# Kernel tuning notes

Hardware: AMD Instinct MI355X
Metric: run time of the kernel (lower is better)

## Reference

```python
import jax, jax.numpy as jnp
import numpy as np

N_NODES = 1_000_000
N_EDGES = 16_000_000
D = 2          # num_dimensions (hard-coded in source)
H = 64         # hidden_channnels
G = 1024       # number of graphs in the batch


def setup_inputs() -> dict:
    key = jax.random.key(0)
    ks = jax.random.split(key, 10)
    x = jax.random.normal(ks[0], (N_NODES, D), dtype=jnp.float32)
    edge_index = jax.random.randint(ks[1], (2, N_EDGES), 0, N_NODES, dtype=jnp.int64)
    batch = jnp.sort(jax.random.randint(ks[2], (N_NODES,), 0, G, dtype=jnp.int64))
    s = 0.5
    return {
        "x": x,
        "lin_w": jax.random.normal(ks[3], (D, D), dtype=jnp.float32) * s,
        "lin_b": jnp.zeros((D,), jnp.float32),
        "gn_weight": jnp.ones((D,), jnp.float32),
        "gn_bias": jnp.zeros((D,), jnp.float32),
        "gn_mean_scale": jnp.ones((D,), jnp.float32),
        "gcn_w": jax.random.normal(ks[4], (D, D), dtype=jnp.float32) * s,
        "gcn_b": jnp.zeros((D,), jnp.float32),
        "fc1_w": jax.random.normal(ks[5], (H, D), dtype=jnp.float32) * s,
        "fc1_b": jnp.zeros((H,), jnp.float32),
        "fc2_w": jax.random.normal(ks[6], (D, H), dtype=jnp.float32) * (1.0 / np.sqrt(H)),
        "fc2_b": jnp.zeros((D,), jnp.float32),
        "edge_index": edge_index,
        "batch": batch,
    }


def reference(x, lin_w, lin_b, gn_weight, gn_bias, gn_mean_scale,
              gcn_w, gcn_b, fc1_w, fc1_b, fc2_w, fc2_b, edge_index, batch):
    n = x.shape[0]
    # lin
    h = x @ lin_w.T + lin_b
    # GraphNorm called without batch -> single-graph stats; eps = num_dimensions = 2 (arg-order quirk)
    mean = h.mean(axis=0)
    out = h - mean * gn_mean_scale
    var = (out * out).mean(axis=0)
    h = gn_weight * out * jax.lax.rsqrt(var + jnp.float32(D)) + gn_bias
    h = jax.nn.relu(h)
    # GCNConv (add_self_loops=True, sym norm) + residual
    row, col = edge_index[0], edge_index[1]
    deg = jax.ops.segment_sum(jnp.ones_like(col, dtype=h.dtype), col, num_segments=n) + 1.0
    dis = jax.lax.rsqrt(deg)                       # deg^{-1/2}
    hw = h @ gcn_w.T                               # [N, D]
    msg = (dis[row] * dis[col])[:, None] * hw[row] # [E, D]
    agg = jax.ops.segment_sum(msg, col, num_segments=n)
    conv = agg + hw / deg[:, None] + gcn_b         # self-loop term = dis_i^2 * hw_i
    h = conv + h
    # fc1
    h = h @ fc1_w.T + fc1_b                        # [N, H]
    # InstanceNorm1d on 2D input -> unbatched (C=N, L=H): per-row norm over H; eps = H (arg-order quirk)
    m = h.mean(axis=1, keepdims=True)
    v = ((h - m) ** 2).mean(axis=1, keepdims=True)
    h = (h - m) * jax.lax.rsqrt(v + jnp.float32(H))
    # fc2
    h = h @ fc2_w.T + fc2_b                        # [N, D]
    # scatter_mean over batch
    ssum = jax.ops.segment_sum(h, batch, num_segments=G)
    cnt = jax.ops.segment_sum(jnp.ones((n,), h.dtype), batch, num_segments=G)
    return ssum / jnp.maximum(cnt, 1.0)[:, None]
```

## Files before the change

kernel.cpp:

```cpp
#include <hip/hip_runtime.h>

#define BLK 256
#define CH 8192
#define BSHIFT 11
#define BRANGE 2048
#define BMASK 2047
#define NSB 512


__global__ void k_stats(const float* __restrict__ x, int n, double* __restrict__ partials) {
    float s0 = 0.f, s1 = 0.f, s2 = 0.f, s3 = 0.f, s4 = 0.f;
    int nv = n >> 1;
    int stride = gridDim.x * blockDim.x;
    for (int i = blockIdx.x * blockDim.x + threadIdx.x; i < nv; i += stride) {
        float4 v = reinterpret_cast<const float4*>(x)[i];
        s0 += v.x + v.z; s1 += v.y + v.w;
        s2 += v.x * v.x + v.z * v.z;
        s3 += v.y * v.y + v.w * v.w;
        s4 += v.x * v.y + v.z * v.w;
    }
    if (blockIdx.x == 0 && threadIdx.x == 0 && (n & 1)) {
        float2 v = reinterpret_cast<const float2*>(x)[n - 1];
        s0 += v.x; s1 += v.y; s2 += v.x * v.x; s3 += v.y * v.y; s4 += v.x * v.y;
    }
    for (int off = 32; off; off >>= 1) {
        s0 += __shfl_down(s0, off);
        s1 += __shfl_down(s1, off);
        s2 += __shfl_down(s2, off);
        s3 += __shfl_down(s3, off);
        s4 += __shfl_down(s4, off);
    }
    __shared__ double lds[4][5];
    int wid = threadIdx.x >> 6;
    if ((threadIdx.x & 63) == 0) {
        lds[wid][0] = s0; lds[wid][1] = s1; lds[wid][2] = s2;
        lds[wid][3] = s3; lds[wid][4] = s4;
    }
    __syncthreads();
    if (threadIdx.x == 0) {
        double t0 = 0, t1 = 0, t2 = 0, t3 = 0, t4 = 0;
        for (int w = 0; w < 4; ++w) {
            t0 += lds[w][0]; t1 += lds[w][1]; t2 += lds[w][2];
            t3 += lds[w][3]; t4 += lds[w][4];
        }
        double* o = partials + (size_t)blockIdx.x * 5;
        o[0] = t0; o[1] = t1; o[2] = t2; o[3] = t3; o[4] = t4;
    }
}


__global__ void k_params(const double* __restrict__ partials, int np,
                         const int* __restrict__ bhist, int NB,
                         int* __restrict__ gbase, int* __restrict__ cursor,
                         const float* lin_w, const float* lin_b,
                         const float* gn_w, const float* gn_b, const float* gn_ms,
                         const float* gcn_w, const float* gcn_b,
                         const float* fc1_w, const float* fc1_b,
                         const float* fc2_w, const float* fc2_b,
                         int n, float* __restrict__ P) {
    int tid = threadIdx.x;
    if (bhist) {
        __shared__ int si[256];
        int v0 = (2 * tid     < NB) ? bhist[2 * tid]     : 0;
        int v1 = (2 * tid + 1 < NB) ? bhist[2 * tid + 1] : 0;
        si[tid] = v0 + v1; __syncthreads();
        for (int off = 1; off < 256; off <<= 1) {
            int t = (tid >= off) ? si[tid - off] : 0;
            __syncthreads();
            si[tid] += t;
            __syncthreads();
        }
        int base = si[tid] - v0 - v1;
        if (2 * tid < NB)     { gbase[2 * tid]     = base;      cursor[2 * tid]     = base; }
        if (2 * tid + 1 < NB) { gbase[2 * tid + 1] = base + v0; cursor[2 * tid + 1] = base + v0; }
        if (tid == 255) gbase[NB] = si[255];
        __syncthreads();
    }
    double a0 = 0, a1 = 0, a2 = 0, a3 = 0, a4 = 0;
    for (int i = tid; i < np; i += blockDim.x) {
        const double* q = partials + (size_t)i * 5;
        a0 += q[0]; a1 += q[1]; a2 += q[2]; a3 += q[3]; a4 += q[4];
    }
    for (int off = 32; off; off >>= 1) {
        a0 += __shfl_down(a0, off);
        a1 += __shfl_down(a1, off);
        a2 += __shfl_down(a2, off);
        a3 += __shfl_down(a3, off);
        a4 += __shfl_down(a4, off);
    }
    __shared__ double red[4][5];
    int wid = tid >> 6;
    if ((tid & 63) == 0) {
        red[wid][0] = a0; red[wid][1] = a1; red[wid][2] = a2;
        red[wid][3] = a3; red[wid][4] = a4;
    }
    __syncthreads();
    if (tid != 0) return;
    double Sx0 = 0, Sx1 = 0, Sxx = 0, Syy = 0, Sxy = 0;
    for (int w = 0; w < 4; ++w) {
        Sx0 += red[w][0]; Sx1 += red[w][1]; Sxx += red[w][2];
        Syy += red[w][3]; Sxy += red[w][4];
    }
    double N = (double)n;
    for (int c = 0; c < 2; ++c) {
        double L0 = lin_w[c * 2], L1 = lin_w[c * 2 + 1], lb = lin_b[c];
        double m   = (L0 * Sx0 + L1 * Sx1) / N + lb;
        double Eh2 = (L0 * L0 * Sxx + L1 * L1 * Syy + 2.0 * L0 * L1 * Sxy
                      + 2.0 * lb * (L0 * Sx0 + L1 * Sx1)) / N + lb * lb;
        double s   = gn_ms[c];
        double var = Eh2 - 2.0 * s * m * m + s * s * m * m;
        double inv = 1.0 / sqrt(var + 2.0);
        double gam = gn_w[c];
        P[c * 2 + 0] = (float)(gam * inv * L0);
        P[c * 2 + 1] = (float)(gam * inv * L1);
        P[4 + c]     = (float)(gam * inv * (lb - m * s) + gn_b[c]);
    }
    P[6] = gcn_w[0]; P[7] = gcn_w[1]; P[8] = gcn_w[2]; P[9] = gcn_w[3];
    P[10] = gcn_b[0]; P[11] = gcn_b[1];
    double b0 = 0, b1 = 0, bb = 0;
    for (int j = 0; j < 64; ++j) { b0 += fc1_w[2 * j]; b1 += fc1_w[2 * j + 1]; bb += fc1_b[j]; }
    b0 /= 64.0; b1 /= 64.0; bb /= 64.0;
    double S00 = 0, S01 = 0, S11 = 0, Sb0 = 0, Sb1 = 0, Sbb = 0;
    double M00 = 0, M01 = 0, M10 = 0, M11 = 0, t0 = 0, t1 = 0;
    for (int j = 0; j < 64; ++j) {
        double w0 = fc1_w[2 * j] - b0, w1 = fc1_w[2 * j + 1] - b1, b = fc1_b[j] - bb;
        S00 += w0 * w0; S01 += w0 * w1; S11 += w1 * w1;
        Sb0 += w0 * b;  Sb1 += w1 * b;  Sbb += b * b;
        double f0 = fc2_w[j], f1 = fc2_w[64 + j];
        M00 += f0 * w0; M01 += f0 * w1; t0 += f0 * b;
        M10 += f1 * w0; M11 += f1 * w1; t1 += f1 * b;
    }
    P[12] = (float)(S00 / 64.0); P[13] = (float)(S01 / 64.0); P[14] = (float)(S11 / 64.0);
    P[15] = (float)(Sb0 / 64.0); P[16] = (float)(Sb1 / 64.0); P[17] = (float)(Sbb / 64.0);
    P[18] = (float)M00; P[19] = (float)M01; P[20] = (float)M10; P[21] = (float)M11;
    P[22] = (float)t0;  P[23] = (float)t1;
    P[24] = fc2_b[0];   P[25] = fc2_b[1];
}


__global__ void k_hist(const int* __restrict__ col, int E, int NB, int* __restrict__ bhist) {
    __shared__ int h[512];
    for (int j = threadIdx.x; j < 512; j += blockDim.x) h[j] = 0;
    __syncthreads();
    int nq = E >> 2;
    int stride = gridDim.x * blockDim.x;
    for (int q = blockIdx.x * blockDim.x + threadIdx.x; q < nq; q += stride) {
        int4 c = reinterpret_cast<const int4*>(col)[q];
        atomicAdd(&h[c.x >> BSHIFT], 1);
        atomicAdd(&h[c.y >> BSHIFT], 1);
        atomicAdd(&h[c.z >> BSHIFT], 1);
        atomicAdd(&h[c.w >> BSHIFT], 1);
    }
    if (blockIdx.x == 0) {
        for (int e = (nq << 2) + threadIdx.x; e < E; e += blockDim.x)
            atomicAdd(&h[col[e] >> BSHIFT], 1);
    }
    __syncthreads();
    for (int j = threadIdx.x; j < NB; j += blockDim.x)
        if (h[j]) atomicAdd(&bhist[j], h[j]);
}

__global__ __launch_bounds__(256) void k_binA(const int* __restrict__ row,
                                              const int* __restrict__ col, int E,
                                              int NB, int* __restrict__ cursor,
                                              unsigned* __restrict__ staging) {
    __shared__ unsigned buf[CH];
    __shared__ int h[512], lpos[512], lcur[512];
    __shared__ int si[256];
    int tid = threadIdx.x;
    int start = blockIdx.x * CH;
    int end = start + CH; if (end > E) end = E;
    h[tid] = 0; h[tid + 256] = 0;
    __syncthreads();
    for (int e = start + tid; e < end; e += 256)
        atomicAdd(&h[col[e] >> BSHIFT], 1);
    __syncthreads();
    int v0 = h[2 * tid], v1 = h[2 * tid + 1];
    si[tid] = v0 + v1; __syncthreads();
    for (int off = 1; off < 256; off <<= 1) {
        int t = (tid >= off) ? si[tid - off] : 0;
        __syncthreads();
        si[tid] += t;
        __syncthreads();
    }
    int base = si[tid] - v0 - v1;
    lpos[2 * tid]     = base;
    lpos[2 * tid + 1] = base + v0;
    lcur[2 * tid]     = (2 * tid     < NB && v0) ? atomicAdd(&cursor[2 * tid],     v0) : 0;
    lcur[2 * tid + 1] = (2 * tid + 1 < NB && v1) ? atomicAdd(&cursor[2 * tid + 1], v1) : 0;
    __syncthreads();
    for (int e = start + tid; e < end; e += 256) {
        int c = col[e];
        unsigned w = ((unsigned)row[e] << BSHIFT) | (unsigned)(c & BMASK);
        int slot = atomicAdd(&lpos[c >> BSHIFT], 1);
        buf[slot] = w;
    }
    __syncthreads();
    int wid = tid >> 6, lane = tid & 63;
    for (int b = wid; b < NB; b += 4) {
        int m = h[b];
        if (!m) continue;
        int lb = lpos[b] - m;
        int g = lcur[b];
        for (int k = lane; k < m; k += 64)
            staging[g + k] = buf[lb + k];
    }
}

__global__ __launch_bounds__(1024) void k_degprep(const unsigned* __restrict__ staging,
                                                  const int* __restrict__ gbase,
                                                  const float* __restrict__ x,
                                                  const float* __restrict__ P,
                                                  int n, int* __restrict__ deg,
                                                  float2* __restrict__ p) {
    __shared__ int hist[BRANGE];
    int tid = threadIdx.x;
    for (int j = tid; j < BRANGE; j += 1024) hist[j] = 0;
    __syncthreads();
    int s = gbase[blockIdx.x], e = gbase[blockIdx.x + 1];
    int pre = (4 - (s & 3)) & 3; int cnt = e - s; if (pre > cnt) pre = cnt;
    for (int i = s + tid; i < s + pre; i += 1024)
        atomicAdd(&hist[staging[i] & BMASK], 1);
    int vs = s + pre;
    int nq = (e - vs) >> 2;
    const uint4* sv = reinterpret_cast<const uint4*>(staging + vs);
    for (int q = tid; q < nq; q += 1024) {
        uint4 w = sv[q];
        atomicAdd(&hist[w.x & BMASK], 1);
        atomicAdd(&hist[w.y & BMASK], 1);
        atomicAdd(&hist[w.z & BMASK], 1);
        atomicAdd(&hist[w.w & BMASK], 1);
    }
    for (int i = vs + (nq << 2) + tid; i < e; i += 1024)
        atomicAdd(&hist[staging[i] & BMASK], 1);
    __syncthreads();
    float A00 = P[0], A01 = P[1], A10 = P[2], A11 = P[3], q0 = P[4], q1 = P[5];
    float g00 = P[6], g01 = P[7], g10 = P[8], g11 = P[9];
    int nb = blockIdx.x << BSHIFT;
    int lim = n - nb; if (lim > BRANGE) lim = BRANGE;
    for (int j = tid; j < lim; j += 1024) {
        int d = hist[j];
        deg[nb + j] = d;
        float2 v = reinterpret_cast<const float2*>(x)[nb + j];
        float gg0 = fmaxf(fmaf(A00, v.x, fmaf(A01, v.y, q0)), 0.f);
        float gg1 = fmaxf(fmaf(A10, v.x, fmaf(A11, v.y, q1)), 0.f);
        float hw0 = g00 * gg0 + g01 * gg1;
        float hw1 = g10 * gg0 + g11 * gg1;
        float degf = (float)d + 1.0f;
        float dis = rsqrtf(degf);
        p[nb + j] = make_float2(dis * hw0, dis * hw1);
    }
}

__global__ __launch_bounds__(1024) void k_aggfin(
        const unsigned* __restrict__ staging, const int* __restrict__ gbase,
        const float2* __restrict__ p, const float* __restrict__ x,
        const int* __restrict__ deg, const int* __restrict__ batch,
        const float* __restrict__ Pp, int n,
        float* __restrict__ gsum, float* __restrict__ gcnt) {
    __shared__ float acc[2 * BRANGE];
    int tid = threadIdx.x;
    for (int j = tid; j < 2 * BRANGE; j += 1024) acc[j] = 0.f;
    __syncthreads();
    int s = gbase[blockIdx.x], e = gbase[blockIdx.x + 1];
    int cnt = e - s;
    int pre = (4 - (s & 3)) & 3; if (pre > cnt) pre = cnt;
    for (int i = s + tid; i < s + pre; i += 1024) {
        unsigned w = staging[i]; float2 pv = p[w >> BSHIFT];
        atomicAdd(&acc[2 * (w & BMASK)],     pv.x);
        atomicAdd(&acc[2 * (w & BMASK) + 1], pv.y);
    }
    int vs = s + pre;
    int nq = (e - vs) >> 2;
    const uint4* sv = reinterpret_cast<const uint4*>(staging + vs);
    #pragma unroll 4
    for (int q = tid; q < nq; q += 1024) {
        uint4 w = sv[q];
        float2 p0 = p[w.x >> BSHIFT], p1 = p[w.y >> BSHIFT];
        float2 p2 = p[w.z >> BSHIFT], p3 = p[w.w >> BSHIFT];
        atomicAdd(&acc[2 * (w.x & BMASK)],     p0.x);
        atomicAdd(&acc[2 * (w.x & BMASK) + 1], p0.y);
        atomicAdd(&acc[2 * (w.y & BMASK)],     p1.x);
        atomicAdd(&acc[2 * (w.y & BMASK) + 1], p1.y);
        atomicAdd(&acc[2 * (w.z & BMASK)],     p2.x);
        atomicAdd(&acc[2 * (w.z & BMASK) + 1], p2.y);
        atomicAdd(&acc[2 * (w.w & BMASK)],     p3.x);
        atomicAdd(&acc[2 * (w.w & BMASK) + 1], p3.y);
    }
    for (int i = vs + (nq << 2) + tid; i < e; i += 1024) {
        unsigned w = staging[i]; float2 pv = p[w >> BSHIFT];
        atomicAdd(&acc[2 * (w & BMASK)],     pv.x);
        atomicAdd(&acc[2 * (w & BMASK) + 1], pv.y);
    }
    __syncthreads();

    float A00 = Pp[0], A01 = Pp[1], A10 = Pp[2], A11 = Pp[3], q0f = Pp[4], q1f = Pp[5];
    float g00 = Pp[6], g01 = Pp[7], g10 = Pp[8], g11 = Pp[9];
    float gb0 = Pp[10], gb1 = Pp[11];
    float S00 = Pp[12], S01 = Pp[13], S11 = Pp[14], Sb0 = Pp[15], Sb1 = Pp[16], Sbb = Pp[17];
    float M00 = Pp[18], M01 = Pp[19], M10 = Pp[20], M11 = Pp[21];
    float t0 = Pp[22], t1 = Pp[23], fb0 = Pp[24], fb1 = Pp[25];
    int nb = blockIdx.x << BSHIFT;
    int lim = n - nb; if (lim > BRANGE) lim = BRANGE;
    for (int j = tid; j < lim; j += 1024) {
        int i = nb + j;
        float2 v = reinterpret_cast<const float2*>(x)[i];
        float g0 = fmaxf(fmaf(A00, v.x, fmaf(A01, v.y, q0f)), 0.f);
        float g1 = fmaxf(fmaf(A10, v.x, fmaf(A11, v.y, q1f)), 0.f);
        float hw0 = g00 * g0 + g01 * g1;
        float hw1 = g10 * g0 + g11 * g1;
        float degf = (float)deg[i] + 1.0f;
        float dis = rsqrtf(degf);
        float a0v = acc[2 * j], a1v = acc[2 * j + 1];
        float c0 = dis * a0v + hw0 / degf + gb0 + g0;
        float c1 = dis * a1v + hw1 / degf + gb1 + g1;
        float vq = S00 * c0 * c0 + 2.f * S01 * c0 * c1 + S11 * c1 * c1
                 + 2.f * Sb0 * c0 + 2.f * Sb1 * c1 + Sbb;
        float inv = rsqrtf(vq + 64.0f);
        float o0 = inv * (M00 * c0 + M01 * c1 + t0) + fb0;
        float o1 = inv * (M10 * c0 + M11 * c1 + t1) + fb1;
        int bg = batch[i];
        unsigned long long act = __ballot(true);
        if (act == ~0ull) {
            int b0 = __shfl(bg, 0);
            if (__all(bg == b0)) {
                float s0 = o0, s1 = o1;
                for (int off = 32; off; off >>= 1) {
                    s0 += __shfl_down(s0, off);
                    s1 += __shfl_down(s1, off);
                }
                if ((tid & 63) == 0) {
                    atomicAdd(&gsum[2 * b0], s0);
                    atomicAdd(&gsum[2 * b0 + 1], s1);
                    atomicAdd(&gcnt[b0], 64.0f);
                }
            } else {
                atomicAdd(&gsum[2 * bg], o0);
                atomicAdd(&gsum[2 * bg + 1], o1);
                atomicAdd(&gcnt[bg], 1.0f);
            }
        } else {
            atomicAdd(&gsum[2 * bg], o0);
            atomicAdd(&gsum[2 * bg + 1], o1);
            atomicAdd(&gcnt[bg], 1.0f);
        }
    }
}

__global__ void k_div(const float* __restrict__ gsum, const float* __restrict__ gcnt,
                      float* __restrict__ out, int G) {
    int g = blockIdx.x * blockDim.x + threadIdx.x;
    if (g < G) {
        float c = fmaxf(gcnt[g], 1.0f);
        out[2 * g]     = gsum[2 * g] / c;
        out[2 * g + 1] = gsum[2 * g + 1] / c;
    }
}


__global__ void k_prep(const float* __restrict__ x, const int* __restrict__ deg,
                       const float* __restrict__ P, int n, float2* __restrict__ p) {
    int stride = gridDim.x * blockDim.x;
    float A00 = P[0], A01 = P[1], A10 = P[2], A11 = P[3], q0 = P[4], q1 = P[5];
    float g00 = P[6], g01 = P[7], g10 = P[8], g11 = P[9];
    for (int i = blockIdx.x * blockDim.x + threadIdx.x; i < n; i += stride) {
        float2 v = reinterpret_cast<const float2*>(x)[i];
        float g0 = fmaxf(fmaf(A00, v.x, fmaf(A01, v.y, q0)), 0.f);
        float g1 = fmaxf(fmaf(A10, v.x, fmaf(A11, v.y, q1)), 0.f);
        float hw0 = g00 * g0 + g01 * g1;
        float hw1 = g10 * g0 + g11 * g1;
        float degf = (float)deg[i] + 1.0f;
        float dis = rsqrtf(degf);
        p[i] = make_float2(dis * hw0, dis * hw1);
    }
}

__global__ void k_deg(const int* __restrict__ col, int E, int* __restrict__ deg) {
    int nq = (E + 3) >> 2;
    int q = blockIdx.x * blockDim.x + threadIdx.x;
    if (q >= nq) return;
    int base = q << 2;
    if (base + 3 < E) {
        int4 c = reinterpret_cast<const int4*>(col)[q];
        atomicAdd(&deg[c.x], 1); atomicAdd(&deg[c.y], 1);
        atomicAdd(&deg[c.z], 1); atomicAdd(&deg[c.w], 1);
    } else {
        for (int e = base; e < E; ++e) atomicAdd(&deg[col[e]], 1);
    }
}

__global__ void k_edge(const int* __restrict__ row, const int* __restrict__ col, int E,
                       const float2* __restrict__ p, float* __restrict__ agg) {
    int nq = (E + 3) >> 2;
    int q = blockIdx.x * blockDim.x + threadIdx.x;
    if (q >= nq) return;
    int base = q << 2;
    if (base + 3 < E) {
        int4 r = reinterpret_cast<const int4*>(row)[q];
        int4 c = reinterpret_cast<const int4*>(col)[q];
        float2 p0 = p[r.x], p1 = p[r.y], p2 = p[r.z], p3 = p[r.w];
        atomicAdd(&agg[2 * c.x], p0.x); atomicAdd(&agg[2 * c.x + 1], p0.y);
        atomicAdd(&agg[2 * c.y], p1.x); atomicAdd(&agg[2 * c.y + 1], p1.y);
        atomicAdd(&agg[2 * c.z], p2.x); atomicAdd(&agg[2 * c.z + 1], p2.y);
        atomicAdd(&agg[2 * c.w], p3.x); atomicAdd(&agg[2 * c.w + 1], p3.y);
    } else {
        for (int e = base; e < E; ++e) {
            float2 pv = p[row[e]];
            atomicAdd(&agg[2 * col[e]], pv.x);
            atomicAdd(&agg[2 * col[e] + 1], pv.y);
        }
    }
}

__global__ void k_final(const float* __restrict__ x, const int* __restrict__ deg,
                        const float* __restrict__ agg, const int* __restrict__ batch,
                        const float* __restrict__ P, int n,
                        float* __restrict__ gsum, float* __restrict__ gcnt) {
    int i = blockIdx.x * blockDim.x + threadIdx.x;
    bool valid = i < n;
    float A00 = P[0], A01 = P[1], A10 = P[2], A11 = P[3], q0 = P[4], q1 = P[5];
    float g00 = P[6], g01 = P[7], g10 = P[8], g11 = P[9];
    float gb0 = P[10], gb1 = P[11];
    float S00 = P[12], S01 = P[13], S11 = P[14], Sb0 = P[15], Sb1 = P[16], Sbb = P[17];
    float M00 = P[18], M01 = P[19], M10 = P[20], M11 = P[21];
    float t0 = P[22], t1 = P[23], fb0 = P[24], fb1 = P[25];

    float o0 = 0.f, o1 = 0.f;
    int b = 0;
    if (valid) {
        float2 v = reinterpret_cast<const float2*>(x)[i];
        float g0 = fmaxf(fmaf(A00, v.x, fmaf(A01, v.y, q0)), 0.f);
        float g1 = fmaxf(fmaf(A10, v.x, fmaf(A11, v.y, q1)), 0.f);
        float hw0 = g00 * g0 + g01 * g1;
        float hw1 = g10 * g0 + g11 * g1;
        float degf = (float)deg[i] + 1.0f;
        float dis = rsqrtf(degf);
        float a0 = agg[2 * i], a1 = agg[2 * i + 1];
        float c0 = dis * a0 + hw0 / degf + gb0 + g0;
        float c1 = dis * a1 + hw1 / degf + gb1 + g1;
        float vq = S00 * c0 * c0 + 2.f * S01 * c0 * c1 + S11 * c1 * c1
                 + 2.f * Sb0 * c0 + 2.f * Sb1 * c1 + Sbb;
        float inv = rsqrtf(vq + 64.0f);
        o0 = inv * (M00 * c0 + M01 * c1 + t0) + fb0;
        o1 = inv * (M10 * c0 + M11 * c1 + t1) + fb1;
        b = batch[i];
    }
    unsigned long long act = __ballot(valid);
    if (act == ~0ull) {
        int b0 = __shfl(b, 0);
        if (__all(b == b0)) {
            float s0 = o0, s1 = o1;
            for (int off = 32; off; off >>= 1) {
                s0 += __shfl_down(s0, off);
                s1 += __shfl_down(s1, off);
            }
            if ((threadIdx.x & 63) == 0) {
                atomicAdd(&gsum[2 * b0], s0);
                atomicAdd(&gsum[2 * b0 + 1], s1);
                atomicAdd(&gcnt[b0], 64.0f);
            }
        } else {
            atomicAdd(&gsum[2 * b], o0);
            atomicAdd(&gsum[2 * b + 1], o1);
            atomicAdd(&gcnt[b], 1.0f);
        }
    } else if (valid) {
        atomicAdd(&gsum[2 * b], o0);
        atomicAdd(&gsum[2 * b + 1], o1);
        atomicAdd(&gcnt[b], 1.0f);
    }
}


extern "C" void kernel_launch(void* const* d_in, const int* in_sizes, int n_in,
                              void* d_out, int out_size, void* d_ws, size_t ws_size,
                              hipStream_t stream) {
    const float* x      = (const float*)d_in[0];
    const float* lin_w  = (const float*)d_in[1];
    const float* lin_b  = (const float*)d_in[2];
    const float* gn_w   = (const float*)d_in[3];
    const float* gn_b   = (const float*)d_in[4];
    const float* gn_ms  = (const float*)d_in[5];
    const float* gcn_w  = (const float*)d_in[6];
    const float* gcn_b  = (const float*)d_in[7];
    const float* fc1_w  = (const float*)d_in[8];
    const float* fc1_b  = (const float*)d_in[9];
    const float* fc2_w  = (const float*)d_in[10];
    const float* fc2_b  = (const float*)d_in[11];
    const int*   ei     = (const int*)d_in[12];
    const int*   batch  = (const int*)d_in[13];

    int n = in_sizes[0] / 2;
    int E = in_sizes[12] / 2;
    int G = out_size / 2;
    const int* row = ei;
    const int* col = ei + E;

    char* ws = (char*)d_ws;
    int nb_nodes = (n + BLK - 1) / BLK;
    int NB = (n + BRANGE - 1) >> BSHIFT;

    size_t zero_end  = 16384 + (size_t)12 * G;
    size_t part_off  = (zero_end + 255) & ~(size_t)255;
    size_t deg_off   = (part_off + (size_t)40 * NSB + 255) & ~(size_t)255;
    size_t p_off     = deg_off + (size_t)4 * n;
    size_t stag_off  = p_off + (size_t)8 * n;
    size_t need      = stag_off + (size_t)4 * E;

    bool fast = (n <= (1 << 20)) && (NB <= 511) && (need <= ws_size) &&
                (zero_end <= 16384 + 12288);

    if (fast) {
        float*    P       = (float*)(ws + 64);
        int*      bhist   = (int*)(ws + 4096);
        int*      gbase   = (int*)(ws + 8192);
        int*      cursor  = (int*)(ws + 12288);
        float*    gsum    = (float*)(ws + 16384);
        float*    gcnt    = (float*)(ws + 16384 + (size_t)8 * G);
        double*   part    = (double*)(ws + part_off);
        int*      deg     = (int*)(ws + deg_off);
        float2*   p       = (float2*)(ws + p_off);
        unsigned* staging = (unsigned*)(ws + stag_off);

        hipMemsetAsync(d_ws, 0, zero_end, stream);

        int nbinA = (E + CH - 1) / CH;

        k_stats<<<NSB, BLK, 0, stream>>>(x, n, part);
        k_hist<<<512, BLK, 0, stream>>>(col, E, NB, bhist);
        k_params<<<1, 256, 0, stream>>>(part, NSB, bhist, NB, gbase, cursor,
                                        lin_w, lin_b, gn_w, gn_b, gn_ms,
                                        gcn_w, gcn_b, fc1_w, fc1_b, fc2_w, fc2_b, n, P);
        k_binA<<<nbinA, 256, 0, stream>>>(row, col, E, NB, cursor, staging);
        k_degprep<<<NB, 1024, 0, stream>>>(staging, gbase, x, P, n, deg, p);
        k_aggfin<<<NB, 1024, 0, stream>>>(staging, gbase, p, x, deg, batch,
                                          P, n, gsum, gcnt);
        k_div<<<(G + BLK - 1) / BLK, BLK, 0, stream>>>(gsum, gcnt, (float*)d_out, G);
    } else {
        float*  P     = (float*)(ws + 64);
        float*  gsum  = (float*)(ws + 4096);
        float*  gcnt  = (float*)(ws + 4096 + (size_t)8 * G);
        size_t fzero_end = 4096 + (size_t)12 * G;
        size_t fpart_off = (fzero_end + 255) & ~(size_t)255;
        size_t fdeg_off  = (fpart_off + (size_t)40 * NSB + 255) & ~(size_t)255;
        int*    deg   = (int*)(ws + fdeg_off);
        size_t fagg_off = fdeg_off + (size_t)4 * n;
        float*  agg   = (float*)(ws + fagg_off);
        size_t fp_off = fagg_off + (size_t)8 * n;
        float2* p     = (float2*)(ws + fp_off);
        double* part  = (double*)(ws + fpart_off);

        hipMemsetAsync(ws + 4096, 0, fzero_end - 4096, stream);
        hipMemsetAsync(ws + fdeg_off, 0, (size_t)12 * n, stream);

        int nq = (E + 3) >> 2;
        int nb_edge = (nq + BLK - 1) / BLK;

        k_stats<<<NSB, BLK, 0, stream>>>(x, n, part);
        k_deg<<<nb_edge, BLK, 0, stream>>>(col, E, deg);
        k_params<<<1, 256, 0, stream>>>(part, NSB, (const int*)nullptr, 0,
                                        (int*)nullptr, (int*)nullptr,
                                        lin_w, lin_b, gn_w, gn_b, gn_ms,
                                        gcn_w, gcn_b, fc1_w, fc1_b, fc2_w, fc2_b, n, P);
        k_prep<<<nb_nodes, BLK, 0, stream>>>(x, deg, P, n, p);
        k_edge<<<nb_edge, BLK, 0, stream>>>(row, col, E, p, agg);
        k_final<<<nb_nodes, BLK, 0, stream>>>(x, deg, agg, batch, P, n, gsum, gcnt);
        k_div<<<(G + BLK - 1) / BLK, BLK, 0, stream>>>(gsum, gcnt, (float*)d_out, G);
    }
}
```

Baseline: 441.4 us.

## Sub-sort each destination bucket's edges by source-row segment to improve gather locality

Within k_degprep, each destination bucket's staged edges are now counted and scattered into eight coarse segments by source row (wave-aggregated atomics), written to a second staging buffer that k_aggfin then consumes. The intent is to make the p[row] gathers in the aggregation kernel more cache-local by visiting source rows in coarse order. It costs an extra read and write of all 16M edge words, a second 4E-byte workspace buffer (disabled if workspace is too small), and many ballots per element. The batch-reduction fast path also drops the full-wave ballot check.

```diff
diff --git a/kernel.cpp b/kernel.cpp
--- a/kernel.cpp
+++ b/kernel.cpp
@@ -207,20 +207,55 @@
     }
 }
 
+__device__ __forceinline__ void seg_count8(int rs, int* segc) {
+    int lane = threadIdx.x & 63;
+    #pragma unroll
+    for (int sgi = 0; sgi < 8; ++sgi) {
+        unsigned long long msk = __ballot(rs == sgi);
+        if (rs == sgi && __popcll(msk & ((1ull << lane) - 1)) == 0)
+            atomicAdd(&segc[sgi], (int)__popcll(msk));
+    }
+}
+
+__device__ __forceinline__ int seg_place8(int rs, int* segcur) {
+    int lane = threadIdx.x & 63;
+    int slot = 0;
+    #pragma unroll
+    for (int sgi = 0; sgi < 8; ++sgi) {
+        unsigned long long msk = __ballot(rs == sgi);
+        if (rs == sgi) {
+            int prel = __popcll(msk & ((1ull << lane) - 1));
+            int src = (int)__ffsll((unsigned long long)msk) - 1;
+            int bse = 0;
+            if (prel == 0) bse = atomicAdd(&segcur[sgi], (int)__popcll(msk));
+            bse = __shfl(bse, src);
+            slot = bse + prel;
+        }
+    }
+    return slot;
+}
+
 __global__ __launch_bounds__(1024) void k_degprep(const unsigned* __restrict__ staging,
                                                   const int* __restrict__ gbase,
                                                   const float* __restrict__ x,
                                                   const float* __restrict__ P,
-                                                  int n, int* __restrict__ deg,
+                                                  int n, int segshift, int do_sort,
+                                                  unsigned* __restrict__ staging2,
+                                                  int* __restrict__ deg,
                                                   float2* __restrict__ p) {
     __shared__ int hist[BRANGE];
+    __shared__ int segc[8];
     int tid = threadIdx.x;
     for (int j = tid; j < BRANGE; j += 1024) hist[j] = 0;
+    if (tid < 8) segc[tid] = 0;
     __syncthreads();
     int s = gbase[blockIdx.x], e = gbase[blockIdx.x + 1];
     int pre = (4 - (s & 3)) & 3; int cnt = e - s; if (pre > cnt) pre = cnt;
-    for (int i = s + tid; i < s + pre; i += 1024)
-        atomicAdd(&hist[staging[i] & BMASK], 1);
+    for (int i = s + tid; i < s + pre; i += 1024) {
+        unsigned w = staging[i];
+        atomicAdd(&hist[w & BMASK], 1);
+        if (do_sort) seg_count8((int)((w >> BSHIFT) >> segshift), segc);
+    }
     int vs = s + pre;
     int nq = (e - vs) >> 2;
     const uint4* sv = reinterpret_cast<const uint4*>(staging + vs);
@@ -230,10 +265,32 @@
         atomicAdd(&hist[w.y & BMASK], 1);
         atomicAdd(&hist[w.z & BMASK], 1);
         atomicAdd(&hist[w.w & BMASK], 1);
-    }
-    for (int i = vs + (nq << 2) + tid; i < e; i += 1024)
-        atomicAdd(&hist[staging[i] & BMASK], 1);
-    __syncthreads();
+        if (do_sort) {
+            seg_count8((int)((w.x >> BSHIFT) >> segshift), segc);
+            seg_count8((int)((w.y >> BSHIFT) >> segshift), segc);
+            seg_count8((int)((w.z >> BSHIFT) >> segshift), segc);
+            seg_count8((int)((w.w >> BSHIFT) >> segshift), segc);
+        }
+    }
+    for (int i = vs + (nq << 2) + tid; i < e; i += 1024) {
+        unsigned w = staging[i];
+        atomicAdd(&hist[w & BMASK], 1);
+        if (do_sort) seg_count8((int)((w >> BSHIFT) >> segshift), segc);
+    }
+    __syncthreads();
+    if (do_sort) {
+        if (tid == 0) {
+            int a = 0;
+            for (int sgi = 0; sgi < 8; ++sgi) { int c = segc[sgi]; segc[sgi] = a; a += c; }
+        }
+        __syncthreads();
+        for (int i = s + tid; i < e; i += 1024) {
+            unsigned w = staging[i];
+            int rs = (int)((w >> BSHIFT) >> segshift);
+            int slot = seg_place8(rs, segc);
+            staging2[s + slot] = w;
+        }
+    }
     float A00 = P[0], A01 = P[1], A10 = P[2], A11 = P[3], q0 = P[4], q1 = P[5];
     float g00 = P[6], g01 = P[7], g10 = P[8], g11 = P[9];
     int nb = blockIdx.x << BSHIFT;
@@ -320,24 +377,17 @@
         float o0 = inv * (M00 * c0 + M01 * c1 + t0) + fb0;
         float o1 = inv * (M10 * c0 + M11 * c1 + t1) + fb1;
         int bg = batch[i];
-        unsigned long long act = __ballot(true);
-        if (act == ~0ull) {
-            int b0 = __shfl(bg, 0);
-            if (__all(bg == b0)) {
-                float s0 = o0, s1 = o1;
-                for (int off = 32; off; off >>= 1) {
-                    s0 += __shfl_down(s0, off);
-                    s1 += __shfl_down(s1, off);
-                }
-                if ((tid & 63) == 0) {
-                    atomicAdd(&gsum[2 * b0], s0);
-                    atomicAdd(&gsum[2 * b0 + 1], s1);
-                    atomicAdd(&gcnt[b0], 64.0f);
-                }
-            } else {
-                atomicAdd(&gsum[2 * bg], o0);
-                atomicAdd(&gsum[2 * bg + 1], o1);
-                atomicAdd(&gcnt[bg], 1.0f);
+        int b0 = __shfl(bg, 0);
+        if (__all(bg == b0)) {
+            float s0 = o0, s1 = o1;
+            for (int off = 32; off; off >>= 1) {
+                s0 += __shfl_down(s0, off);
+                s1 += __shfl_down(s1, off);
+            }
+            if ((tid & 63) == 0) {
+                atomicAdd(&gsum[2 * b0], s0);
+                atomicAdd(&gsum[2 * b0 + 1], s1);
+                atomicAdd(&gcnt[b0], 64.0f);
             }
         } else {
             atomicAdd(&gsum[2 * bg], o0);
@@ -500,27 +550,35 @@
     int nb_nodes = (n + BLK - 1) / BLK;
     int NB = (n + BRANGE - 1) >> BSHIFT;
 
+    int segshift = 0;
+    while (((unsigned)(n - 1) >> segshift) > 7u) ++segshift;
+
     size_t zero_end  = 16384 + (size_t)12 * G;
     size_t part_off  = (zero_end + 255) & ~(size_t)255;
     size_t deg_off   = (part_off + (size_t)40 * NSB + 255) & ~(size_t)255;
     size_t p_off     = deg_off + (size_t)4 * n;
     size_t stag_off  = p_off + (size_t)8 * n;
-    size_t need      = stag_off + (size_t)4 * E;
+    size_t stag2_off = stag_off + (size_t)4 * E;
+    size_t need      = stag2_off + (size_t)4 * E;
+
+    int do_sort = 1;
+    if (need > ws_size) { do_sort = 0; need = stag_off + (size_t)4 * E; }
 
     bool fast = (n <= (1 << 20)) && (NB <= 511) && (need <= ws_size) &&
                 (zero_end <= 16384 + 12288);
 
     if (fast) {
-        float*    P       = (float*)(ws + 64);
-        int*      bhist   = (int*)(ws + 4096);
-        int*      gbase   = (int*)(ws + 8192);
-        int*      cursor  = (int*)(ws + 12288);
-        float*    gsum    = (float*)(ws + 16384);
-        float*    gcnt    = (float*)(ws + 16384 + (size_t)8 * G);
-        double*   part    = (double*)(ws + part_off);
-        int*      deg     = (int*)(ws + deg_off);
-        float2*   p       = (float2*)(ws + p_off);
-        unsigned* staging = (unsigned*)(ws + stag_off);
+        float*    P        = (float*)(ws + 64);
+        int*      bhist    = (int*)(ws + 4096);
+        int*      gbase    = (int*)(ws + 8192);
+        int*      cursor   = (int*)(ws + 12288);
+        float*    gsum     = (float*)(ws + 16384);
+        float*    gcnt     = (float*)(ws + 16384 + (size_t)8 * G);
+        double*   part     = (double*)(ws + part_off);
+        int*      deg      = (int*)(ws + deg_off);
+        float2*   p        = (float2*)(ws + p_off);
+        unsigned* staging  = (unsigned*)(ws + stag_off);
+        unsigned* staging2 = do_sort ? (unsigned*)(ws + stag2_off) : (unsigned*)(ws + stag_off);
 
         hipMemsetAsync(d_ws, 0, zero_end, stream);
 
@@ -532,8 +590,9 @@
                                         lin_w, lin_b, gn_w, gn_b, gn_ms,
                                         gcn_w, gcn_b, fc1_w, fc1_b, fc2_w, fc2_b, n, P);
         k_binA<<<nbinA, 256, 0, stream>>>(row, col, E, NB, cursor, staging);
-        k_degprep<<<NB, 1024, 0, stream>>>(staging, gbase, x, P, n, deg, p);
-        k_aggfin<<<NB, 1024, 0, stream>>>(staging, gbase, p, x, deg, batch,
+        k_degprep<<<NB, 1024, 0, stream>>>(staging, gbase, x, P, n, segshift, do_sort,
+                                           staging2, deg, p);
+        k_aggfin<<<NB, 1024, 0, stream>>>(staging2, gbase, p, x, deg, batch,
                                           P, n, gsum, gcnt);
         k_div<<<(G + BLK - 1) / BLK, BLK, 0, stream>>>(gsum, gcnt, (float*)d_out, G);
     } else {
```

Measured after the change: 557.8 us. +26.4%, slower.
